# Optimization experiments

Measured on AMD Instinct MI355X. Metric: run time of the kernel, lower is better.

## Reference

```python
import jax, jax.numpy as jnp
import numpy as np

B, S, D = 4, 4096, 64

def setup_inputs() -> dict:
    key = jax.random.key(0)
    kq, kk, kv = jax.random.split(key, 3)
    q = jax.random.normal(kq, (B, S, D), dtype=jnp.float32)
    k = jax.random.normal(kk, (B, S, D), dtype=jnp.float32)
    v = jax.random.normal(kv, (B, S, D), dtype=jnp.float32)
    return {"q": q, "k": k, "v": v}

def reference(q, k, v):
    d_k = k.shape[-1]
    # scores: [B, S, S]
    scores = jnp.einsum('bqd,bkd->bqk', q, k) / jnp.sqrt(jnp.asarray(d_k, q.dtype))
    s = scores.shape[-1]
    # causal mask: disallow j > i (strict upper triangle)
    causal = jnp.tril(jnp.ones((scores.shape[-2], s), dtype=bool))
    scores = jnp.where(causal, scores, jnp.asarray(-jnp.inf, scores.dtype))
    norm_scores = jax.nn.softmax(scores, axis=-1)
    return jnp.einsum('bqk,bkd->bqd', norm_scores, v)
```

## Files before the change

kernel.cpp:

```cpp
#include <hip/hip_runtime.h>

#define B_ 4
#define S_ 4096
#define D_ 64

typedef __attribute__((ext_vector_type(8))) short short8;
typedef __attribute__((ext_vector_type(4))) float f32x4;
typedef __attribute__((ext_vector_type(16))) float f32x16;
typedef __attribute__((ext_vector_type(4))) int int4v;
typedef __attribute__((ext_vector_type(2))) unsigned uint2v;
typedef unsigned short u16;

__device__ __forceinline__ unsigned pack_bf2(float a, float b) {
  unsigned ua = __float_as_uint(a) + 0x8000u;
  unsigned ub = __float_as_uint(b) + 0x8000u;
  return __builtin_amdgcn_perm(ub, ua, 0x07060302);
}

__device__ __forceinline__ uint2v permswap(unsigned a, unsigned b) {
#if __has_builtin(__builtin_amdgcn_permlane32_swap)
  return __builtin_amdgcn_permlane32_swap(a, b, false, false);
#else
  int h = (threadIdx.x >> 5) & 1;
  unsigned ta = __shfl_xor(a, 32);
  unsigned tb = __shfl_xor(b, 32);
  uint2v r;
  r[0] = h ? tb : a;
  r[1] = h ? b : ta;
  return r;
#endif
}

__global__ __launch_bounds__(256) void cvt_all_k(const float* __restrict__ q,
                                                 const float* __restrict__ k,
                                                 const float* __restrict__ v,
                                                 u16* __restrict__ wsQ,
                                                 u16* __restrict__ wsK,
                                                 u16* __restrict__ wsV) {
  int blk = blockIdx.x;
  if (blk < 1024) {
    const float* src = (blk < 512) ? q : k;
    u16* dst = (blk < 512) ? wsQ : wsK;
    float scale = (blk < 512) ? 0.18033688011112042f : 1.0f;
    int t = ((blk & 511) << 8) + threadIdx.x;
    const f32x4* s4 = (const f32x4*)src;
    f32x4 a = s4[2 * t], b = s4[2 * t + 1];
    int4v r;
    r[0] = (int)pack_bf2(a[0] * scale, a[1] * scale);
    r[1] = (int)pack_bf2(a[2] * scale, a[3] * scale);
    r[2] = (int)pack_bf2(b[0] * scale, b[1] * scale);
    r[3] = (int)pack_bf2(b[2] * scale, b[3] * scale);
    *(int4v*)(dst + 8 * (long)t) = r;
  } else {
    int t = ((blk - 1024) << 8) + threadIdx.x;
    int lane = t & 63;
    int J  = (t >> 6) & 3;
    int dt = (t >> 8) & 1;
    int ck = (t >> 9) & 63;
    int b  = t >> 15;
    int row = ck * 64 + J * 16 + (lane >> 5) * 8;
    int col = dt * 32 + (lane & 31);
    const float* src = v + ((long)(b * S_ + row)) * D_ + col;
    float e[8];
#pragma unroll
    for (int i = 0; i < 8; i++) e[i] = src[(long)i * D_];
    int4v r;
    r[0] = (int)pack_bf2(e[0], e[1]);
    r[1] = (int)pack_bf2(e[2], e[3]);
    r[2] = (int)pack_bf2(e[4], e[5]);
    r[3] = (int)pack_bf2(e[6], e[7]);
    *(int4v*)(wsV + 8 * (long)t) = r;
  }
}

#define MFMA32(a, bb, cc) __builtin_amdgcn_mfma_f32_32x32x16_bf16((a), (bb), (cc), 0, 0, 0)

__global__ __launch_bounds__(512, 2) void attn_k(const u16* __restrict__ wsQ,
                                                 const u16* __restrict__ wsK,
                                                 const u16* __restrict__ wsV,
                                                 float* __restrict__ out) {
  int bid = blockIdx.x;
  int b   = bid & 3;
  int g32 = 127 - (bid >> 2);
  int tid = threadIdx.x;
  int w = tid >> 6, lane = tid & 63, c2 = lane & 31, h = lane >> 5;
  int cmax = g32 >> 1;
  int q0 = g32 * 32;

  __shared__ float sMem[8][2176];
  __shared__ float sML[8][32];

  float* W = &sMem[w][0];

  short8 qf[4];
#pragma unroll
  for (int kk = 0; kk < 4; kk++)
    qf[kk] = *(const short8*)(wsQ + ((long)(b * S_ + q0 + c2)) * D_ + kk * 16 + h * 8);

  f32x16 o0, o1;
#pragma unroll
  for (int r = 0; r < 16; r++) { o0[r] = 0.f; o1[r] = 0.f; }
  float lp = 0.f;

  for (int ck = w; ck <= cmax; ck += 8) {
    const u16* kp = wsK + ((long)(b * S_ + ck * 64 + c2)) * D_ + h * 8;
    short8 kf[2][4];
#pragma unroll
    for (int jt = 0; jt < 2; jt++)
#pragma unroll
      for (int kk = 0; kk < 4; kk++)
        kf[jt][kk] = *(const short8*)(kp + jt * 32 * D_ + kk * 16);
    const u16* vp = wsV + ((long)(b * 64 + ck)) * 4096 + (long)lane * 8;
    short8 vf[2][4];
#pragma unroll
    for (int dt = 0; dt < 2; dt++)
#pragma unroll
      for (int J = 0; J < 4; J++)
        vf[dt][J] = *(const short8*)(vp + (dt * 4 + J) * 512);

    f32x16 s[2];
#pragma unroll
    for (int r = 0; r < 16; r++) { s[0][r] = 0.f; s[1][r] = 0.f; }
#pragma unroll
    for (int kk = 0; kk < 4; kk++) {
      s[0] = MFMA32(kf[0][kk], qf[kk], s[0]);
      s[1] = MFMA32(kf[1][kk], qf[kk], s[1]);
    }

    if (ck == cmax) {
      int dq = 32 * (g32 & 1) + c2;
#pragma unroll
      for (int r = 0; r < 16; r++) {
        int row = (r & 3) + 8 * (r >> 2) + 4 * h;
        if (row      > dq) s[0][r] = -1e30f;
        if (row + 32 > dq) s[1][r] = -1e30f;
      }
    }

    float sum = 0.f;
#pragma unroll
    for (int r = 0; r < 16; r++) {
      s[0][r] = exp2f(s[0][r]); sum += s[0][r];
      s[1][r] = exp2f(s[1][r]); sum += s[1][r];
    }
    lp += sum;

    short8 p[4];
#pragma unroll
    for (int jt = 0; jt < 2; jt++) {
      unsigned D[8];
#pragma unroll
      for (int g = 0; g < 4; g++) {
        D[2 * g]     = pack_bf2(s[jt][4 * g],     s[jt][4 * g + 1]);
        D[2 * g + 1] = pack_bf2(s[jt][4 * g + 2], s[jt][4 * g + 3]);
      }
#pragma unroll
      for (int e = 0; e < 2; e++) {
        uint2v r0 = permswap(D[4 * e],     D[4 * e + 2]);
        uint2v r1 = permswap(D[4 * e + 1], D[4 * e + 3]);
        int4v pw;
        pw[0] = (int)r0[0]; pw[1] = (int)r1[0];
        pw[2] = (int)r0[1]; pw[3] = (int)r1[1];
        p[2 * jt + e] = __builtin_bit_cast(short8, pw);
      }
    }

#pragma unroll
    for (int J = 0; J < 4; J++) {
      o0 = MFMA32(vf[0][J], p[J], o0);
      o1 = MFMA32(vf[1][J], p[J], o1);
    }
  }

  lp += __shfl_xor(lp, 32);
  if (h == 0) sML[w][c2] = lp;
#pragma unroll
  for (int dt = 0; dt < 2; dt++)
#pragma unroll
    for (int grp = 0; grp < 4; grp++) {
      f32x4 t4;
      const f32x16& ov = dt ? o1 : o0;
      t4[0] = ov[4 * grp]; t4[1] = ov[4 * grp + 1];
      t4[2] = ov[4 * grp + 2]; t4[3] = ov[4 * grp + 3];
      *(f32x4*)&W[c2 * 68 + 32 * dt + 8 * grp + 4 * h] = t4;
    }
  __syncthreads();

  int q = tid >> 4, d4 = tid & 15;
  float L = 0.f;
  f32x4 acc = {0.f, 0.f, 0.f, 0.f};
#pragma unroll
  for (int w2 = 0; w2 < 8; w2++) {
    L += sML[w2][q];
    f32x4 pv = *(f32x4*)&sMem[w2][q * 68 + d4 * 4];
#pragma unroll
    for (int i = 0; i < 4; i++) acc[i] += pv[i];
  }
  float inv = 1.f / L;
  f32x4 r;
#pragma unroll
  for (int i = 0; i < 4; i++) r[i] = acc[i] * inv;
  *(f32x4*)(out + ((long)(b * S_ + q0 + q)) * D_ + d4 * 4) = r;
}

extern "C" void kernel_launch(void* const* d_in, const int* in_sizes, int n_in,
                              void* d_out, int out_size, void* d_ws, size_t ws_size,
                              hipStream_t stream) {
  const float* q = (const float*)d_in[0];
  const float* k = (const float*)d_in[1];
  const float* v = (const float*)d_in[2];
  float* out = (float*)d_out;

  u16* wsQ = (u16*)d_ws;
  u16* wsK = wsQ + (long)B_ * S_ * D_;
  u16* wsV = wsK + (long)B_ * S_ * D_;

  cvt_all_k<<<1536, 256, 0, stream>>>(q, k, v, wsQ, wsK, wsV);
  attn_k<<<512, 512, 0, stream>>>(wsQ, wsK, wsV, out);
}
```

Baseline: 93.00 us.

## Process 64 query rows per block to reuse K/V fragments across two query tiles

Each block now handles 64 queries (two 32-row tiles) instead of 32, so every K and V chunk loaded from memory feeds twice the MFMA work. The grid is halved to 256 blocks, and the cross-wave reduction runs twice through the same shared buffer with an extra barrier. This raises register pressure (four output accumulators plus two Q fragment sets) and halves the block count, which may hurt occupancy and load balance on a chip with many CUs.

```diff
diff --git a/kernel.cpp b/kernel.cpp
--- a/kernel.cpp
+++ b/kernel.cpp
@@ -81,26 +81,30 @@
                                                  float* __restrict__ out) {
   int bid = blockIdx.x;
   int b   = bid & 3;
-  int g32 = 127 - (bid >> 2);
+  int g64 = 63 - (bid >> 2);
   int tid = threadIdx.x;
   int w = tid >> 6, lane = tid & 63, c2 = lane & 31, h = lane >> 5;
-  int cmax = g32 >> 1;
-  int q0 = g32 * 32;
+  int cmax = g64;
+  int q0 = g64 * 64;
 
   __shared__ float sMem[8][2176];
-  __shared__ float sML[8][32];
+  __shared__ float sML[8][64];
 
   float* W = &sMem[w][0];
 
-  short8 qf[4];
-#pragma unroll
-  for (int kk = 0; kk < 4; kk++)
-    qf[kk] = *(const short8*)(wsQ + ((long)(b * S_ + q0 + c2)) * D_ + kk * 16 + h * 8);
-
-  f32x16 o0, o1;
-#pragma unroll
-  for (int r = 0; r < 16; r++) { o0[r] = 0.f; o1[r] = 0.f; }
-  float lp = 0.f;
+  short8 qf[2][4];
+#pragma unroll
+  for (int tq = 0; tq < 2; tq++)
+#pragma unroll
+    for (int kk = 0; kk < 4; kk++)
+      qf[tq][kk] = *(const short8*)(wsQ + ((long)(b * S_ + q0 + tq * 32 + c2)) * D_ + kk * 16 + h * 8);
+
+  f32x16 o[4];
+#pragma unroll
+  for (int t = 0; t < 4; t++)
+#pragma unroll
+    for (int r = 0; r < 16; r++) o[t][r] = 0.f;
+  float lp0 = 0.f, lp1 = 0.f;
 
   for (int ck = w; ck <= cmax; ck += 8) {
     const u16* kp = wsK + ((long)(b * S_ + ck * 64 + c2)) * D_ + h * 8;
@@ -118,89 +122,98 @@
       for (int J = 0; J < 4; J++)
         vf[dt][J] = *(const short8*)(vp + (dt * 4 + J) * 512);
 
-    f32x16 s[2];
-#pragma unroll
-    for (int r = 0; r < 16; r++) { s[0][r] = 0.f; s[1][r] = 0.f; }
-#pragma unroll
-    for (int kk = 0; kk < 4; kk++) {
-      s[0] = MFMA32(kf[0][kk], qf[kk], s[0]);
-      s[1] = MFMA32(kf[1][kk], qf[kk], s[1]);
-    }
-
-    if (ck == cmax) {
-      int dq = 32 * (g32 & 1) + c2;
+#pragma unroll
+    for (int tq = 0; tq < 2; tq++) {
+      f32x16 s[2];
+#pragma unroll
+      for (int r = 0; r < 16; r++) { s[0][r] = 0.f; s[1][r] = 0.f; }
+#pragma unroll
+      for (int kk = 0; kk < 4; kk++) {
+        s[0] = MFMA32(kf[0][kk], qf[tq][kk], s[0]);
+        s[1] = MFMA32(kf[1][kk], qf[tq][kk], s[1]);
+      }
+
+      if (ck == cmax) {
+        int dq = 32 * tq + c2;
+#pragma unroll
+        for (int r = 0; r < 16; r++) {
+          int row = (r & 3) + 8 * (r >> 2) + 4 * h;
+          if (row      > dq) s[0][r] = -1e30f;
+          if (row + 32 > dq) s[1][r] = -1e30f;
+        }
+      }
+
+      float sum = 0.f;
 #pragma unroll
       for (int r = 0; r < 16; r++) {
-        int row = (r & 3) + 8 * (r >> 2) + 4 * h;
-        if (row      > dq) s[0][r] = -1e30f;
-        if (row + 32 > dq) s[1][r] = -1e30f;
-      }
-    }
-
-    float sum = 0.f;
-#pragma unroll
-    for (int r = 0; r < 16; r++) {
-      s[0][r] = exp2f(s[0][r]); sum += s[0][r];
-      s[1][r] = exp2f(s[1][r]); sum += s[1][r];
-    }
-    lp += sum;
-
-    short8 p[4];
-#pragma unroll
-    for (int jt = 0; jt < 2; jt++) {
-      unsigned D[8];
-#pragma unroll
-      for (int g = 0; g < 4; g++) {
-        D[2 * g]     = pack_bf2(s[jt][4 * g],     s[jt][4 * g + 1]);
-        D[2 * g + 1] = pack_bf2(s[jt][4 * g + 2], s[jt][4 * g + 3]);
-      }
-#pragma unroll
-      for (int e = 0; e < 2; e++) {
-        uint2v r0 = permswap(D[4 * e],     D[4 * e + 2]);
-        uint2v r1 = permswap(D[4 * e + 1], D[4 * e + 3]);
-        int4v pw;
-        pw[0] = (int)r0[0]; pw[1] = (int)r1[0];
-        pw[2] = (int)r0[1]; pw[3] = (int)r1[1];
-        p[2 * jt + e] = __builtin_bit_cast(short8, pw);
-      }
-    }
-
-#pragma unroll
-    for (int J = 0; J < 4; J++) {
-      o0 = MFMA32(vf[0][J], p[J], o0);
-      o1 = MFMA32(vf[1][J], p[J], o1);
+        s[0][r] = exp2f(s[0][r]); sum += s[0][r];
+        s[1][r] = exp2f(s[1][r]); sum += s[1][r];
+      }
+      if (tq) lp1 += sum; else lp0 += sum;
+
+      short8 p[4];
+#pragma unroll
+      for (int jt = 0; jt < 2; jt++) {
+        unsigned Dw[8];
+#pragma unroll
+        for (int g = 0; g < 4; g++) {
+          Dw[2 * g]     = pack_bf2(s[jt][4 * g],     s[jt][4 * g + 1]);
+          Dw[2 * g + 1] = pack_bf2(s[jt][4 * g + 2], s[jt][4 * g + 3]);
+        }
+#pragma unroll
+        for (int e = 0; e < 2; e++) {
+          uint2v r0 = permswap(Dw[4 * e],     Dw[4 * e + 2]);
+          uint2v r1 = permswap(Dw[4 * e + 1], Dw[4 * e + 3]);
+          int4v pw;
+          pw[0] = (int)r0[0]; pw[1] = (int)r1[0];
+          pw[2] = (int)r0[1]; pw[3] = (int)r1[1];
+          p[2 * jt + e] = __builtin_bit_cast(short8, pw);
+        }
+      }
+
+#pragma unroll
+      for (int J = 0; J < 4; J++) {
+        o[2 * tq + 0] = MFMA32(vf[0][J], p[J], o[2 * tq + 0]);
+        o[2 * tq + 1] = MFMA32(vf[1][J], p[J], o[2 * tq + 1]);
+      }
     }
   }
 
-  lp += __shfl_xor(lp, 32);
-  if (h == 0) sML[w][c2] = lp;
-#pragma unroll
-  for (int dt = 0; dt < 2; dt++)
-#pragma unroll
-    for (int grp = 0; grp < 4; grp++) {
-      f32x4 t4;
-      const f32x16& ov = dt ? o1 : o0;
-      t4[0] = ov[4 * grp]; t4[1] = ov[4 * grp + 1];
-      t4[2] = ov[4 * grp + 2]; t4[3] = ov[4 * grp + 3];
-      *(f32x4*)&W[c2 * 68 + 32 * dt + 8 * grp + 4 * h] = t4;
+  lp0 += __shfl_xor(lp0, 32);
+  lp1 += __shfl_xor(lp1, 32);
+  if (h == 0) { sML[w][c2] = lp0; sML[w][32 + c2] = lp1; }
+
+#pragma unroll
+  for (int tq = 0; tq < 2; tq++) {
+    if (tq) __syncthreads();
+#pragma unroll
+    for (int dt = 0; dt < 2; dt++)
+#pragma unroll
+      for (int grp = 0; grp < 4; grp++) {
+        f32x4 t4;
+        const f32x16& ov = o[2 * tq + dt];
+        t4[0] = ov[4 * grp]; t4[1] = ov[4 * grp + 1];
+        t4[2] = ov[4 * grp + 2]; t4[3] = ov[4 * grp + 3];
+        *(f32x4*)&W[c2 * 68 + 32 * dt + 8 * grp + 4 * h] = t4;
+      }
+    __syncthreads();
+
+    int q = tid >> 4, d4 = tid & 15;
+    float L = 0.f;
+    f32x4 acc = {0.f, 0.f, 0.f, 0.f};
+#pragma unroll
+    for (int w2 = 0; w2 < 8; w2++) {
+      L += sML[w2][tq * 32 + q];
+      f32x4 pv = *(f32x4*)&sMem[w2][q * 68 + d4 * 4];
+#pragma unroll
+      for (int i = 0; i < 4; i++) acc[i] += pv[i];
     }
-  __syncthreads();
-
-  int q = tid >> 4, d4 = tid & 15;
-  float L = 0.f;
-  f32x4 acc = {0.f, 0.f, 0.f, 0.f};
-#pragma unroll
-  for (int w2 = 0; w2 < 8; w2++) {
-    L += sML[w2][q];
-    f32x4 pv = *(f32x4*)&sMem[w2][q * 68 + d4 * 4];
-#pragma unroll
-    for (int i = 0; i < 4; i++) acc[i] += pv[i];
+    float inv = 1.f / L;
+    f32x4 r;
+#pragma unroll
+    for (int i = 0; i < 4; i++) r[i] = acc[i] * inv;
+    *(f32x4*)(out + ((long)(b * S_ + q0 + tq * 32 + q)) * D_ + d4 * 4) = r;
   }
-  float inv = 1.f / L;
-  f32x4 r;
-#pragma unroll
-  for (int i = 0; i < 4; i++) r[i] = acc[i] * inv;
-  *(f32x4*)(out + ((long)(b * S_ + q0 + q)) * D_ + d4 * 4) = r;
 }
 
 extern "C" void kernel_launch(void* const* d_in, const int* in_sizes, int n_in,
@@ -216,5 +229,5 @@
   u16* wsV = wsK + (long)B_ * S_ * D_;
 
   cvt_all_k<<<1536, 256, 0, stream>>>(q, k, v, wsQ, wsK, wsV);
-  attn_k<<<512, 512, 0, stream>>>(wsQ, wsK, wsV, out);
-}
+  attn_k<<<256, 512, 0, stream>>>(wsQ, wsK, wsV, out);
+}
```

New measurement: 98.50 us. 1.06x slower.
